# Kernel tuning notes

Hardware: AMD Instinct MI355X
Metric: run time of the kernel (lower is better)

The kernel has to match this reference:

```python
import jax, jax.numpy as jnp
import numpy as np

B, N, DIM = 2, 4096, 1024
HEADS, DH = 16, 64
W = 512                       # window_size; look_backward=1, look_forward=0 (causal)
INNER = HEADS * DH            # 1024
FF_INNER = int(DIM * 4 * 2 / 3)  # 2730, GEGLU inner dim
MASK_VAL = -1e9


def setup_inputs() -> dict:
    key = jax.random.key(0)
    ks = jax.random.split(key, 6)
    s = 0.02
    return {
        "x": jax.random.normal(ks[0], (B, N, DIM), jnp.float32),
        "mask": jnp.ones((B, N), jnp.bool_),
        "ln1_w": jnp.ones((DIM,), jnp.float32),
        "ln1_b": jnp.zeros((DIM,), jnp.float32),
        "w_qkv": jax.random.normal(ks[1], (DIM, 3 * INNER), jnp.float32) * s,
        "w_out": jax.random.normal(ks[2], (INNER, DIM), jnp.float32) * s,
        "ln2_w": jnp.ones((DIM,), jnp.float32),
        "ln2_b": jnp.zeros((DIM,), jnp.float32),
        "w_ff1": jax.random.normal(ks[3], (DIM, 2 * FF_INNER), jnp.float32) * s,
        "w_ff2": jax.random.normal(ks[4], (FF_INNER, DIM), jnp.float32) * s,
    }


def layer_norm(x, w, b, eps=1e-5):
    mu = x.mean(-1, keepdims=True)
    var = ((x - mu) ** 2).mean(-1, keepdims=True)
    return (x - mu) * jax.lax.rsqrt(var + eps) * w + b


def look_around(t, pad_value):
    # t: (..., nw, w, ...) over axis=-3/-2 layout (b?, nw, w, d?) handled by caller.
    # prepend previous window along the window axis (axis=-3 for 5D k/v, axis=0 for positions)
    return t


def local_attention(q, k, v, mask):
    # q,k,v: [b, h, n, d]; causal sliding-window attention, look_backward=1,
    # exact_windowsize=True (each query sees exactly the previous W positions + itself).
    b, h, n, d = q.shape
    nw = n // W
    scale = d ** -0.5
    qw = q.reshape(b, h, nw, W, d) * scale
    kw = k.reshape(b, h, nw, W, d)
    vw = v.reshape(b, h, nw, W, d)

    # look_around: concat previous window (zeros for window 0) -> keys of size 2W
    def prev(t):
        return jnp.pad(t, ((0, 0), (0, 0), (1, 0), (0, 0), (0, 0)))[:, :, :-1]
    k2 = jnp.concatenate([prev(kw), kw], axis=3)  # [b,h,nw,2W,d]
    v2 = jnp.concatenate([prev(vw), vw], axis=3)

    # absolute positions; pad windows get index -1
    t_pos = jnp.arange(n).reshape(nw, W)
    t_prev = jnp.pad(t_pos, ((1, 0), (0, 0)), constant_values=-1)[:-1]
    bq_t = t_pos                                  # [nw, W]
    bk_t = jnp.concatenate([t_prev, t_pos], axis=-1)  # [nw, 2W]

    pad_mask = bk_t == -1                                       # [nw,2W]
    causal_mask = bq_t[:, :, None] < bk_t[:, None, :]           # key after query
    exact_mask = bq_t[:, :, None] > (bk_t[:, None, :] + W)      # beyond window (look_backward*W)
    invalid = pad_mask[:, None, :] | causal_mask | exact_mask   # [nw,W,2W]

    # key padding mask from input mask
    mw = mask.reshape(b, nw, W)
    m_prev = jnp.pad(mw, ((0, 0), (1, 0), (0, 0)), constant_values=False)[:, :-1]
    mk = jnp.concatenate([m_prev, mw], axis=-1)                 # [b,nw,2W]

    sim = jnp.einsum('bhnid,bhnjd->bhnij', qw, k2)              # [b,h,nw,W,2W]
    bad = invalid[None, None] | (~mk)[:, None, :, None, :]
    sim = jnp.where(bad, MASK_VAL, sim)
    attn = jax.nn.softmax(sim, axis=-1)
    out = jnp.einsum('bhnij,bhnjd->bhnid', attn, v2)
    return out.reshape(b, h, n, d)


def reference(x, mask, ln1_w, ln1_b, w_qkv, w_out, ln2_w, ln2_b, w_ff1, w_ff2):
    b, n, _ = x.shape
    # ---- LocalMHA (prenorm) ----
    h = layer_norm(x, ln1_w, ln1_b)
    qkv = h @ w_qkv                                   # [b,n,3*inner]
    q, k, v = jnp.split(qkv, 3, axis=-1)
    def to_heads(t):
        return t.reshape(b, n, HEADS, DH).transpose(0, 2, 1, 3)  # b h n d
    q, k, v = to_heads(q), to_heads(k), to_heads(v)
    o = local_attention(q, k, v, mask)
    o = o.transpose(0, 2, 1, 3).reshape(b, n, INNER)
    x = x + o @ w_out
    # ---- GEGLU FeedForward (prenorm via LayerNorm in Sequential) ----
    h2 = layer_norm(x, ln2_w, ln2_b)
    u = h2 @ w_ff1
    a, gate = jnp.split(u, 2, axis=-1)
    ff = (a * jax.nn.gelu(gate, approximate=False)) @ w_ff2
    return x + ff
```

## Files before the change

### kernel.cpp

```cpp
#include <hip/hip_runtime.h>
#include <cstdint>


#define DEVI __device__ __forceinline__

typedef __bf16 bf16x8 __attribute__((ext_vector_type(8)));
typedef float f32x4 __attribute__((ext_vector_type(4)));

typedef __attribute__((address_space(1))) void gvoid_t;
typedef __attribute__((address_space(3))) void lvoid_t;

DEVI void gld16(const void* g, void* l) {
  __builtin_amdgcn_global_load_lds((gvoid_t*)g, (lvoid_t*)l, 16, 0, 0);
}

DEVI unsigned short f2bf(float f) {
  union { float f; unsigned int u; } c; c.f = f;
  unsigned int u = c.u;
  return (unsigned short)((u + 0x7fffu + ((u >> 16) & 1u)) >> 16);
}

DEVI float fexp2(float x) {
#if __has_builtin(__builtin_amdgcn_exp2f)
  return __builtin_amdgcn_exp2f(x);
#else
  return exp2f(x);
#endif
}

DEVI f32x4 mfma16(bf16x8 a, bf16x8 b, f32x4 c) {
  return __builtin_amdgcn_mfma_f32_16x16x32_bf16(a, b, c, 0, 0, 0);
}

__global__ __launch_bounds__(256) void wtrans_k(
    const float* __restrict__ W, int K, int strideW, int colOff, int Ncols,
    unsigned short* __restrict__ WT, int KC)
{
  __shared__ float tile[32][33];
  const int tx = threadIdx.x & 31, ty = threadIdx.x >> 5;
  const int kb = blockIdx.x * 32, nb = blockIdx.y * 32;
#pragma unroll
  for (int i = 0; i < 4; ++i) {
    const int k = kb + ty + i * 8, n = nb + tx;
    float v = 0.f;
    if (k < K && n < Ncols) v = W[(size_t)k * strideW + colOff + n];
    tile[ty + i * 8][tx] = v;
  }
  __syncthreads();
#pragma unroll
  for (int i = 0; i < 4; ++i) {
    const int n = nb + ty + i * 8, k = kb + tx;
    WT[(size_t)n * KC + k] = f2bf(tile[tx][ty + i * 8]);
  }
}

__global__ __launch_bounds__(256) void ln_k(
    const float* __restrict__ x, const float* __restrict__ w,
    const float* __restrict__ b, unsigned short* __restrict__ out)
{
  const int wid = threadIdx.x >> 6, lane = threadIdx.x & 63;
  const int row = blockIdx.x * 4 + wid;
  const float* xr = x + (size_t)row * 1024;
  float v[16];
  float s = 0.f;
#pragma unroll
  for (int i = 0; i < 16; ++i) { v[i] = xr[lane + i * 64]; s += v[i]; }
#pragma unroll
  for (int off = 32; off > 0; off >>= 1) s += __shfl_xor(s, off, 64);
  const float mu = s * (1.f / 1024.f);
  float s2 = 0.f;
#pragma unroll
  for (int i = 0; i < 16; ++i) { const float d = v[i] - mu; s2 += d * d; }
#pragma unroll
  for (int off = 32; off > 0; off >>= 1) s2 += __shfl_xor(s2, off, 64);
  const float rs = rsqrtf(s2 * (1.f / 1024.f) + 1e-5f);
#pragma unroll
  for (int i = 0; i < 16; ++i) {
    const int c = lane + i * 64;
    out[(size_t)row * 1024 + c] = f2bf((v[i] - mu) * rs * w[c] + b[c]);
  }
}

__global__ __launch_bounds__(256) void vtrans_k(
    const unsigned short* __restrict__ qkv, unsigned short* __restrict__ vT)
{
  __shared__ __attribute__((aligned(16))) unsigned short tile[64 * 72];
  const int bh = blockIdx.x, tt = blockIdx.y;
  const int b = bh >> 4, hh = bh & 15;
  const int tid = threadIdx.x;
#pragma unroll
  for (int i = 0; i < 2; ++i) {
    const int ch = tid + i * 256;
    const int t = ch >> 3, dc = ch & 7;
    const uint4 val = *(const uint4*)
        &qkv[((size_t)(b * 4096 + tt * 64 + t)) * 3072 + 2048 + hh * 64 + dc * 8];
    *(uint4*)&tile[t * 72 + dc * 8] = val;
  }
  __syncthreads();
#pragma unroll
  for (int i = 0; i < 2; ++i) {
    const int ch = tid + i * 256;
    const int d = ch >> 3, tc = ch & 7;
    union { unsigned short u[8]; uint4 v; } pk;
#pragma unroll
    for (int j = 0; j < 8; ++j) pk.u[j] = tile[(tc * 8 + j) * 72 + d];
    *(uint4*)&vT[((size_t)(bh * 64 + d)) * 4096 + tt * 64 + tc * 8] = pk.v;
  }
}

template <int EPI>
__global__ __launch_bounds__(256, 2) void gemm_k(
    const unsigned short* __restrict__ A, const unsigned short* __restrict__ BT,
    const unsigned short* __restrict__ BT2, const float* __restrict__ resid,
    void* __restrict__ outp, int M, int N, int K)
{
  __shared__ __attribute__((aligned(16))) unsigned short Asm[128 * 32];
  __shared__ __attribute__((aligned(16))) unsigned short Bsm[128 * 32];
  __shared__ __attribute__((aligned(16))) unsigned short B2sm[(EPI == 2) ? 128 * 32 : 8];
  const int tid = threadIdx.x;
  const int wid = tid >> 6, lane = tid & 63;
  const int wy = wid >> 1, wx = wid & 1;
  const int lr = lane & 15, quad = lane >> 4;
  const int m0 = blockIdx.y * 128, n0 = blockIdx.x * 128;

  f32x4 acc[4][4] = {};
  f32x4 acc2[4][4] = {};

  for (int k0 = 0; k0 < K; k0 += 32) {
    __syncthreads();
#pragma unroll
    for (int iss = 0; iss < 2; ++iss) {
      const int ch = iss * 256 + wid * 64 + lane;
      const int row = ch >> 2, kc = ch & 3;
      const int ldsoff = (iss * 256 + wid * 64) * 8;
      gld16(&A[(size_t)(m0 + row) * K + k0 + kc * 8], &Asm[ldsoff]);
      gld16(&BT[(size_t)(n0 + row) * K + k0 + kc * 8], &Bsm[ldsoff]);
      if (EPI == 2)
        gld16(&BT2[(size_t)(n0 + row) * K + k0 + kc * 8], &B2sm[ldsoff]);
    }
    __syncthreads();

    bf16x8 af[4], bfr[4], b2f[4];
#pragma unroll
    for (int t = 0; t < 4; ++t) {
      af[t]  = *(const bf16x8*)&Asm[(wy * 64 + t * 16 + lr) * 32 + quad * 8];
      bfr[t] = *(const bf16x8*)&Bsm[(wx * 64 + t * 16 + lr) * 32 + quad * 8];
      if (EPI == 2)
        b2f[t] = *(const bf16x8*)&B2sm[(wx * 64 + t * 16 + lr) * 32 + quad * 8];
    }
#pragma unroll
    for (int mt = 0; mt < 4; ++mt)
#pragma unroll
      for (int nt = 0; nt < 4; ++nt) {
        acc[mt][nt] = mfma16(af[mt], bfr[nt], acc[mt][nt]);
        if (EPI == 2) acc2[mt][nt] = mfma16(af[mt], b2f[nt], acc2[mt][nt]);
      }
  }

#pragma unroll
  for (int mt = 0; mt < 4; ++mt)
#pragma unroll
    for (int nt = 0; nt < 4; ++nt)
#pragma unroll
      for (int r = 0; r < 4; ++r) {
        const int row = m0 + wy * 64 + mt * 16 + quad * 4 + r;
        const int col = n0 + wx * 64 + nt * 16 + lr;
        const size_t idx = (size_t)row * N + col;
        if (EPI == 0) {
          ((unsigned short*)outp)[idx] = f2bf(acc[mt][nt][r]);
        } else if (EPI == 1) {
          ((float*)outp)[idx] = acc[mt][nt][r] + resid[idx];
        } else {
          const float a = acc[mt][nt][r];
          const float g = acc2[mt][nt][r];
          const float ge = 0.5f * g * (1.0f + erff(g * 0.70710678118654752f));
          ((unsigned short*)outp)[idx] = f2bf(a * ge);
        }
      }
}

__global__ __launch_bounds__(64, 2) void attn_k(
    const unsigned short* __restrict__ qkv, const unsigned short* __restrict__ vT,
    unsigned short* __restrict__ o)
{
  __shared__ __attribute__((aligned(16))) unsigned short Ksm[64 * 64];
  __shared__ __attribute__((aligned(16))) unsigned short Vsm[64 * 64];
  __shared__ __attribute__((aligned(16))) unsigned short Psm[64 * 72];

  const int bx = blockIdx.x;
  const int qt = bx & 63, hh = (bx >> 6) & 15, b = bx >> 10;
  const int bhead = bx >> 6;
  const int lane = threadIdx.x & 63;
  const int lr = lane & 15, quad = lane >> 4;
  const int q0 = qt * 64;
  const size_t rowB = (size_t)b * 4096;
  const float scale2 = 0.18033688011112042f;

  bf16x8 qf[4][2];
#pragma unroll
  for (int mt = 0; mt < 4; ++mt)
#pragma unroll
    for (int ks = 0; ks < 2; ++ks)
      qf[mt][ks] = *(const bf16x8*)
          &qkv[(rowB + q0 + mt * 16 + lr) * 3072 + hh * 64 + ks * 32 + quad * 8];

  f32x4 O[4][4] = {};
  float lS[4][4] = {};

  const int kstart = (q0 >= 512) ? (q0 - 512) : 0;
  const int ntiles = (q0 + 64 - kstart) >> 6;

  for (int kt = 0; kt < ntiles; ++kt) {
    const int k0t = kstart + kt * 64;
    __syncthreads();
#pragma unroll
    for (int i = 0; i < 8; ++i) {
      gld16(&qkv[(rowB + k0t + i * 8 + (lane >> 3)) * 3072 + 1024 + hh * 64 + (lane & 7) * 8],
            &Ksm[i * 512]);
      gld16(&vT[((size_t)(bhead * 64 + i * 8 + (lane >> 3))) * 4096 + k0t + (lane & 7) * 8],
            &Vsm[i * 512]);
    }
    __syncthreads();

    f32x4 S[4][4];
    bf16x8 kf[4][2];
#pragma unroll
    for (int nt = 0; nt < 4; ++nt)
#pragma unroll
      for (int ks = 0; ks < 2; ++ks)
        kf[nt][ks] = *(const bf16x8*)&Ksm[(nt * 16 + lr) * 64 + ks * 32 + quad * 8];
#pragma unroll
    for (int mt = 0; mt < 4; ++mt)
#pragma unroll
      for (int nt = 0; nt < 4; ++nt) {
        f32x4 z = {};
        z = mfma16(qf[mt][0], kf[nt][0], z);
        S[mt][nt] = mfma16(qf[mt][1], kf[nt][1], z);
      }

#pragma unroll
    for (int mt = 0; mt < 4; ++mt)
#pragma unroll
      for (int nt = 0; nt < 4; ++nt)
#pragma unroll
        for (int r = 0; r < 4; ++r) {
          const int qpos = q0 + mt * 16 + quad * 4 + r;
          const int kpos = k0t + nt * 16 + lr;
          const bool bad = (kpos > qpos) || (kpos < qpos - 512);
          const float p = bad ? 0.f : fexp2(S[mt][nt][r] * scale2);
          lS[mt][r] += p;
          Psm[(mt * 16 + quad * 4 + r) * 72 + nt * 16 + lr] = f2bf(p);
        }

    bf16x8 vf[4][2];
#pragma unroll
    for (int dt = 0; dt < 4; ++dt)
#pragma unroll
      for (int jt = 0; jt < 2; ++jt)
        vf[dt][jt] = *(const bf16x8*)&Vsm[(dt * 16 + lr) * 64 + jt * 32 + quad * 8];
#pragma unroll
    for (int mt = 0; mt < 4; ++mt)
#pragma unroll
      for (int jt = 0; jt < 2; ++jt) {
        const bf16x8 pf = *(const bf16x8*)&Psm[(mt * 16 + lr) * 72 + jt * 32 + quad * 8];
#pragma unroll
        for (int dt = 0; dt < 4; ++dt)
          O[mt][dt] = mfma16(pf, vf[dt][jt], O[mt][dt]);
      }
  }

#pragma unroll
  for (int mt = 0; mt < 4; ++mt)
#pragma unroll
    for (int r = 0; r < 4; ++r) {
      float s = lS[mt][r];
#pragma unroll
      for (int off = 1; off < 16; off <<= 1) s += __shfl_xor(s, off, 64);
      lS[mt][r] = 1.f / s;
    }

#pragma unroll
  for (int mt = 0; mt < 4; ++mt)
#pragma unroll
    for (int dt = 0; dt < 4; ++dt)
#pragma unroll
      for (int r = 0; r < 4; ++r) {
        const int row = q0 + mt * 16 + quad * 4 + r;
        o[(rowB + row) * 1024 + hh * 64 + dt * 16 + lr] = f2bf(O[mt][dt][r] * lS[mt][r]);
      }
}

extern "C" void kernel_launch(void* const* d_in, const int* in_sizes, int n_in,
                              void* d_out, int out_size, void* d_ws, size_t ws_size,
                              hipStream_t stream)
{
  (void)in_sizes; (void)n_in; (void)out_size; (void)ws_size;
  const float* x    = (const float*)d_in[0];
  const float* ln1w = (const float*)d_in[2];
  const float* ln1b = (const float*)d_in[3];
  const float* wqkv = (const float*)d_in[4];
  const float* wout = (const float*)d_in[5];
  const float* ln2w = (const float*)d_in[6];
  const float* ln2b = (const float*)d_in[7];
  const float* wff1 = (const float*)d_in[8];
  const float* wff2 = (const float*)d_in[9];

  char* p = (char*)d_ws;
  auto alloc = [&](size_t n) { char* r = p; p += (n + 255) & ~(size_t)255; return r; };
  unsigned short* wT_qkv = (unsigned short*)alloc(3072ull * 1024 * 2);
  unsigned short* wT_out = (unsigned short*)alloc(1024ull * 1024 * 2);
  unsigned short* wTa    = (unsigned short*)alloc(2816ull * 1024 * 2);
  unsigned short* wTg    = (unsigned short*)alloc(2816ull * 1024 * 2);
  unsigned short* wT_ff2 = (unsigned short*)alloc(1024ull * 2816 * 2);
  unsigned short* bufX   = (unsigned short*)alloc(8192ull * 1024 * 2);
  unsigned short* qkvg   = (unsigned short*)alloc(8192ull * 3072 * 2);
  unsigned short* obuf   = (unsigned short*)alloc(8192ull * 1024 * 2);
  float*          x1     = (float*)alloc(8192ull * 1024 * 4);

  wtrans_k<<<dim3(32, 96), 256, 0, stream>>>(wqkv, 1024, 3072, 0, 3072, wT_qkv, 1024);
  wtrans_k<<<dim3(32, 32), 256, 0, stream>>>(wout, 1024, 1024, 0, 1024, wT_out, 1024);
  wtrans_k<<<dim3(32, 88), 256, 0, stream>>>(wff1, 1024, 5460, 0,    2730, wTa, 1024);
  wtrans_k<<<dim3(32, 88), 256, 0, stream>>>(wff1, 1024, 5460, 2730, 2730, wTg, 1024);
  wtrans_k<<<dim3(88, 32), 256, 0, stream>>>(wff2, 2730, 1024, 0,   1024, wT_ff2, 2816);

  ln_k<<<dim3(2048), 256, 0, stream>>>(x, ln1w, ln1b, bufX);
  gemm_k<0><<<dim3(24, 64), 256, 0, stream>>>(bufX, wT_qkv, nullptr, nullptr,
                                              (void*)qkvg, 8192, 3072, 1024);
  vtrans_k<<<dim3(32, 64), 256, 0, stream>>>(qkvg, bufX);
  attn_k<<<dim3(2048), 64, 0, stream>>>(qkvg, bufX, obuf);
  gemm_k<1><<<dim3(8, 64), 256, 0, stream>>>(obuf, wT_out, nullptr, x,
                                             (void*)x1, 8192, 1024, 1024);
  ln_k<<<dim3(2048), 256, 0, stream>>>(x1, ln2w, ln2b, bufX);
  gemm_k<2><<<dim3(22, 64), 256, 0, stream>>>(bufX, wTa, wTg, nullptr,
                                              (void*)qkvg, 8192, 2816, 1024);
  gemm_k<1><<<dim3(8, 64), 256, 0, stream>>>(qkvg, wT_ff2, nullptr, x1,
                                             d_out, 8192, 1024, 2816);
}
```

Baseline: 549.3 us.

## Split GEGLU into dedicated kernel, raise GEMM occupancy, merge weight transposes

Merges the five weight-transpose launches into one kernel that dispatches on block index. Moves the GEGLU dual-GEMM into its own kernel with a 128x64 output tile and a single shared LDS buffer, which halves the accumulator registers per thread. This allows launch bounds of 3 blocks per CU for both GEMM kernels. The goal is to cut launch overhead and raise occupancy. The cost is that the A tile is now re-read across twice as many N-blocks in the GEGLU GEMM.

```diff
diff --git a/kernel.cpp b/kernel.cpp
--- a/kernel.cpp
+++ b/kernel.cpp
@@ -32,13 +32,38 @@
   return __builtin_amdgcn_mfma_f32_16x16x32_bf16(a, b, c, 0, 0, 0);
 }
 
-__global__ __launch_bounds__(256) void wtrans_k(
-    const float* __restrict__ W, int K, int strideW, int colOff, int Ncols,
-    unsigned short* __restrict__ WT, int KC)
+__global__ __launch_bounds__(256) void wtrans_all_k(
+    const float* __restrict__ wqkv, const float* __restrict__ wout,
+    const float* __restrict__ wff1, const float* __restrict__ wff2,
+    unsigned short* __restrict__ wT_qkv, unsigned short* __restrict__ wT_out,
+    unsigned short* __restrict__ wTa, unsigned short* __restrict__ wTg,
+    unsigned short* __restrict__ wT_ff2)
 {
   __shared__ float tile[32][33];
+  int idx = blockIdx.x;
+  const float* W; unsigned short* WT;
+  int K, strideW, colOff, Ncols, KC, kb, nb;
+  if (idx < 3072) {
+    W = wqkv; WT = wT_qkv; K = 1024; strideW = 3072; colOff = 0; Ncols = 3072; KC = 1024;
+    kb = (idx & 31) * 32; nb = (idx >> 5) * 32;
+  } else if (idx < 4096) {
+    idx -= 3072;
+    W = wout; WT = wT_out; K = 1024; strideW = 1024; colOff = 0; Ncols = 1024; KC = 1024;
+    kb = (idx & 31) * 32; nb = (idx >> 5) * 32;
+  } else if (idx < 6912) {
+    idx -= 4096;
+    W = wff1; WT = wTa; K = 1024; strideW = 5460; colOff = 0; Ncols = 2730; KC = 1024;
+    kb = (idx & 31) * 32; nb = (idx >> 5) * 32;
+  } else if (idx < 9728) {
+    idx -= 6912;
+    W = wff1; WT = wTg; K = 1024; strideW = 5460; colOff = 2730; Ncols = 2730; KC = 1024;
+    kb = (idx & 31) * 32; nb = (idx >> 5) * 32;
+  } else {
+    idx -= 9728;
+    W = wff2; WT = wT_ff2; K = 2730; strideW = 1024; colOff = 0; Ncols = 1024; KC = 2816;
+    kb = (idx % 88) * 32; nb = (idx / 88) * 32;
+  }
   const int tx = threadIdx.x & 31, ty = threadIdx.x >> 5;
-  const int kb = blockIdx.x * 32, nb = blockIdx.y * 32;
 #pragma unroll
   for (int i = 0; i < 4; ++i) {
     const int k = kb + ty + i * 8, n = nb + tx;
@@ -109,14 +134,12 @@
 }
 
 template <int EPI>
-__global__ __launch_bounds__(256, 2) void gemm_k(
+__global__ __launch_bounds__(256, 3) void gemm_k(
     const unsigned short* __restrict__ A, const unsigned short* __restrict__ BT,
-    const unsigned short* __restrict__ BT2, const float* __restrict__ resid,
-    void* __restrict__ outp, int M, int N, int K)
+    const float* __restrict__ resid, void* __restrict__ outp, int M, int N, int K)
 {
   __shared__ __attribute__((aligned(16))) unsigned short Asm[128 * 32];
   __shared__ __attribute__((aligned(16))) unsigned short Bsm[128 * 32];
-  __shared__ __attribute__((aligned(16))) unsigned short B2sm[(EPI == 2) ? 128 * 32 : 8];
   const int tid = threadIdx.x;
   const int wid = tid >> 6, lane = tid & 63;
   const int wy = wid >> 1, wx = wid & 1;
@@ -124,7 +147,6 @@
   const int m0 = blockIdx.y * 128, n0 = blockIdx.x * 128;
 
   f32x4 acc[4][4] = {};
-  f32x4 acc2[4][4] = {};
 
   for (int k0 = 0; k0 < K; k0 += 32) {
     __syncthreads();
@@ -135,26 +157,20 @@
       const int ldsoff = (iss * 256 + wid * 64) * 8;
       gld16(&A[(size_t)(m0 + row) * K + k0 + kc * 8], &Asm[ldsoff]);
       gld16(&BT[(size_t)(n0 + row) * K + k0 + kc * 8], &Bsm[ldsoff]);
-      if (EPI == 2)
-        gld16(&BT2[(size_t)(n0 + row) * K + k0 + kc * 8], &B2sm[ldsoff]);
-    }
-    __syncthreads();
-
-    bf16x8 af[4], bfr[4], b2f[4];
+    }
+    __syncthreads();
+
+    bf16x8 af[4], bfr[4];
 #pragma unroll
     for (int t = 0; t < 4; ++t) {
       af[t]  = *(const bf16x8*)&Asm[(wy * 64 + t * 16 + lr) * 32 + quad * 8];
       bfr[t] = *(const bf16x8*)&Bsm[(wx * 64 + t * 16 + lr) * 32 + quad * 8];
-      if (EPI == 2)
-        b2f[t] = *(const bf16x8*)&B2sm[(wx * 64 + t * 16 + lr) * 32 + quad * 8];
     }
 #pragma unroll
     for (int mt = 0; mt < 4; ++mt)
 #pragma unroll
-      for (int nt = 0; nt < 4; ++nt) {
+      for (int nt = 0; nt < 4; ++nt)
         acc[mt][nt] = mfma16(af[mt], bfr[nt], acc[mt][nt]);
-        if (EPI == 2) acc2[mt][nt] = mfma16(af[mt], b2f[nt], acc2[mt][nt]);
-      }
   }
 
 #pragma unroll
@@ -168,14 +184,77 @@
         const size_t idx = (size_t)row * N + col;
         if (EPI == 0) {
           ((unsigned short*)outp)[idx] = f2bf(acc[mt][nt][r]);
-        } else if (EPI == 1) {
+        } else {
           ((float*)outp)[idx] = acc[mt][nt][r] + resid[idx];
-        } else {
-          const float a = acc[mt][nt][r];
-          const float g = acc2[mt][nt][r];
-          const float ge = 0.5f * g * (1.0f + erff(g * 0.70710678118654752f));
-          ((unsigned short*)outp)[idx] = f2bf(a * ge);
         }
+      }
+}
+
+__global__ __launch_bounds__(256, 3) void geglu_k(
+    const unsigned short* __restrict__ A, const unsigned short* __restrict__ BTa,
+    const unsigned short* __restrict__ BTg, unsigned short* __restrict__ outp,
+    int M, int N, int K)
+{
+  __shared__ __attribute__((aligned(16))) unsigned short S[8192];
+  const int tid = threadIdx.x;
+  const int wid = tid >> 6, lane = tid & 63;
+  const int wy = wid >> 1, wx = wid & 1;
+  const int lr = lane & 15, quad = lane >> 4;
+  const int m0 = blockIdx.y * 128, n0 = blockIdx.x * 64;
+
+  f32x4 acc_a[4][2] = {};
+  f32x4 acc_g[4][2] = {};
+
+  for (int k0 = 0; k0 < K; k0 += 32) {
+    __syncthreads();
+#pragma unroll
+    for (int iss = 0; iss < 4; ++iss) {
+      const int ch = iss * 256 + wid * 64 + lane;
+      const int ldsoff = (iss * 256 + wid * 64) * 8;
+      const void* g;
+      if (ch < 512) {
+        g = &A[(size_t)(m0 + (ch >> 2)) * K + k0 + (ch & 3) * 8];
+      } else if (ch < 768) {
+        const int c = ch - 512;
+        g = &BTa[(size_t)(n0 + (c >> 2)) * K + k0 + (c & 3) * 8];
+      } else {
+        const int c = ch - 768;
+        g = &BTg[(size_t)(n0 + (c >> 2)) * K + k0 + (c & 3) * 8];
+      }
+      gld16(g, &S[ldsoff]);
+    }
+    __syncthreads();
+
+    bf16x8 af[4], ba[2], bg[2];
+#pragma unroll
+    for (int t = 0; t < 4; ++t)
+      af[t] = *(const bf16x8*)&S[(wy * 64 + t * 16 + lr) * 32 + quad * 8];
+#pragma unroll
+    for (int t = 0; t < 2; ++t) {
+      ba[t] = *(const bf16x8*)&S[4096 + (wx * 32 + t * 16 + lr) * 32 + quad * 8];
+      bg[t] = *(const bf16x8*)&S[6144 + (wx * 32 + t * 16 + lr) * 32 + quad * 8];
+    }
+#pragma unroll
+    for (int mt = 0; mt < 4; ++mt)
+#pragma unroll
+      for (int nt = 0; nt < 2; ++nt) {
+        acc_a[mt][nt] = mfma16(af[mt], ba[nt], acc_a[mt][nt]);
+        acc_g[mt][nt] = mfma16(af[mt], bg[nt], acc_g[mt][nt]);
+      }
+  }
+
+#pragma unroll
+  for (int mt = 0; mt < 4; ++mt)
+#pragma unroll
+    for (int nt = 0; nt < 2; ++nt)
+#pragma unroll
+      for (int r = 0; r < 4; ++r) {
+        const int row = m0 + wy * 64 + mt * 16 + quad * 4 + r;
+        const int col = n0 + wx * 32 + nt * 16 + lr;
+        const float a = acc_a[mt][nt][r];
+        const float g = acc_g[mt][nt][r];
+        const float ge = 0.5f * g * (1.0f + erff(g * 0.70710678118654752f));
+        outp[(size_t)row * N + col] = f2bf(a * ge);
       }
 }
 
@@ -317,22 +396,17 @@
   unsigned short* obuf   = (unsigned short*)alloc(8192ull * 1024 * 2);
   float*          x1     = (float*)alloc(8192ull * 1024 * 4);
 
-  wtrans_k<<<dim3(32, 96), 256, 0, stream>>>(wqkv, 1024, 3072, 0, 3072, wT_qkv, 1024);
-  wtrans_k<<<dim3(32, 32), 256, 0, stream>>>(wout, 1024, 1024, 0, 1024, wT_out, 1024);
-  wtrans_k<<<dim3(32, 88), 256, 0, stream>>>(wff1, 1024, 5460, 0,    2730, wTa, 1024);
-  wtrans_k<<<dim3(32, 88), 256, 0, stream>>>(wff1, 1024, 5460, 2730, 2730, wTg, 1024);
-  wtrans_k<<<dim3(88, 32), 256, 0, stream>>>(wff2, 2730, 1024, 0,   1024, wT_ff2, 2816);
-
+  wtrans_all_k<<<dim3(12544), 256, 0, stream>>>(wqkv, wout, wff1, wff2,
+                                                wT_qkv, wT_out, wTa, wTg, wT_ff2);
   ln_k<<<dim3(2048), 256, 0, stream>>>(x, ln1w, ln1b, bufX);
-  gemm_k<0><<<dim3(24, 64), 256, 0, stream>>>(bufX, wT_qkv, nullptr, nullptr,
+  gemm_k<0><<<dim3(24, 64), 256, 0, stream>>>(bufX, wT_qkv, nullptr,
                                               (void*)qkvg, 8192, 3072, 1024);
   vtrans_k<<<dim3(32, 64), 256, 0, stream>>>(qkvg, bufX);
   attn_k<<<dim3(2048), 64, 0, stream>>>(qkvg, bufX, obuf);
-  gemm_k<1><<<dim3(8, 64), 256, 0, stream>>>(obuf, wT_out, nullptr, x,
+  gemm_k<1><<<dim3(8, 64), 256, 0, stream>>>(obuf, wT_out, x,
                                              (void*)x1, 8192, 1024, 1024);
   ln_k<<<dim3(2048), 256, 0, stream>>>(x1, ln2w, ln2b, bufX);
-  gemm_k<2><<<dim3(22, 64), 256, 0, stream>>>(bufX, wTa, wTg, nullptr,
-                                              (void*)qkvg, 8192, 2816, 1024);
-  gemm_k<1><<<dim3(8, 64), 256, 0, stream>>>(qkvg, wT_ff2, nullptr, x1,
+  geglu_k<<<dim3(44, 64), 256, 0, stream>>>(bufX, wTa, wTg, qkvg, 8192, 2816, 1024);
+  gemm_k<1><<<dim3(8, 64), 256, 0, stream>>>(qkvg, wT_ff2, x1,
                                              d_out, 8192, 1024, 2816);
 }
```

Result: no change. 546.5 us (-0.5%).
